# Performance work log

Hardware: AMD Instinct MI355X
Metric: run time of the kernel (lower is better)

Reference implementation:

```python
import jax, jax.numpy as jnp
import numpy as np

B, S_F, S_H, S_W = 1, 4, 32, 32
S = S_F * S_H * S_W            # 4096 video tokens
DIM, HEADS = 1536, 12
HD = DIM // HEADS              # 128
EPS = 1e-6


def _rope_angles(max_pos, dim_half):
    inv = 1.0 / (10000.0 ** (np.arange(dim_half, dtype=np.float32) / dim_half))
    return (np.arange(max_pos, dtype=np.float32)[:, None] * inv[None, :]).astype(np.float32)


def setup_inputs():
    key = jax.random.key(0)
    ks = jax.random.split(key, 6)
    w = lambda k: jax.random.normal(k, (DIM, DIM), jnp.float32) * (DIM ** -0.5)
    c = HD // 2
    f0, f1 = c - 2 * (c // 3), c // 3   # 22, 21 (Wan rope split for F/H/W)
    freqs = jnp.asarray(np.concatenate(
        [_rope_angles(1024, f0), _rope_angles(1024, f1), _rope_angles(1024, f1)], axis=1))
    return dict(
        x=jax.random.normal(ks[0], (B, S, DIM), jnp.float32),
        seq_lens=jnp.full((B,), S, jnp.int32),
        grid_sizes=jnp.array([[S_F, S_H, S_W]], jnp.int32),
        freqs=freqs,
        t=500,
        Wq=w(ks[1]), bq=jnp.zeros((DIM,), jnp.float32),
        Wk=w(ks[2]), bk=jnp.zeros((DIM,), jnp.float32),
        Wv=w(ks[3]), bv=jnp.zeros((DIM,), jnp.float32),
        Wo=w(ks[4]), bo=jnp.zeros((DIM,), jnp.float32),
        gq=jnp.ones((DIM,), jnp.float32),
        gk=jnp.ones((DIM,), jnp.float32),
    )


def _rmsnorm(x, g):
    return x * jax.lax.rsqrt(jnp.mean(x * x, axis=-1, keepdims=True) + EPS) * g


def _rope_apply(x, cos, sin):
    # x: [B,S,n,d]; cos/sin: [S, d//2]; rotate interleaved (even, odd) pairs
    b, s, n, d = x.shape
    xr = x.reshape(b, s, n, d // 2, 2)
    xe, xo = xr[..., 0], xr[..., 1]
    c = cos[None, :, None, :]
    sn = sin[None, :, None, :]
    return jnp.stack([xe * c - xo * sn, xe * sn + xo * c], axis=-1).reshape(b, s, n, d)


def _rope_tables(grid_sizes, freqs):
    F, H, W = [int(v) for v in np.asarray(grid_sizes)[0]]
    c = HD // 2
    f0, f1 = c - 2 * (c // 3), c // 3
    ang = jnp.concatenate([
        jnp.broadcast_to(freqs[:F, :f0][:, None, None, :], (F, H, W, f0)),
        jnp.broadcast_to(freqs[:H, f0:f0 + f1][None, :, None, :], (F, H, W, f1)),
        jnp.broadcast_to(freqs[:W, f0 + f1:][None, None, :, :], (F, H, W, f1)),
    ], axis=-1).reshape(F * H * W, c)  # [S, d//2]
    return jnp.cos(ang), jnp.sin(ang)


def reference(x, seq_lens, grid_sizes, freqs, t, Wq, bq, Wk, bk, Wv, bv, Wo, bo, gq, gk):
    b, s = x.shape[:2]
    cos, sin = _rope_tables(grid_sizes, freqs)

    q = _rmsnorm(x @ Wq.T + bq, gq).reshape(b, s, HEADS, HD)
    k = _rmsnorm(x @ Wk.T + bk, gk).reshape(b, s, HEADS, HD)
    v = (x @ Wv.T + bv).reshape(b, s, HEADS, HD)
    q = _rope_apply(q, cos, sin)
    k = _rope_apply(k, cos, sin)

    scores = jnp.einsum('bqhd,bkhd->bhqk', q, k) * (HD ** -0.5)  # [B,H,S,S]
    kmask = jnp.arange(s)[None, :] < seq_lens[:, None]           # varlen key mask
    scores = jnp.where(kmask[:, None, None, :], scores, -jnp.inf)
    attn = jax.nn.softmax(scores, axis=-1)
    out = jnp.einsum('bhqk,bkhd->bqhd', attn, v).reshape(b, s, DIM)
    return out @ Wo.T + bo
```

## Files before the change

kernel.cpp:

```cpp
#include <hip/hip_runtime.h>
#include <hip/hip_bf16.h>

#define S 4096
#define DIM 1536
#define HEADS 12
#define HD 128
#define CHALF 64
#define NQKV 4608

typedef unsigned short u16;
typedef unsigned int u32;
typedef __attribute__((ext_vector_type(8))) short bf16x8;
typedef __attribute__((ext_vector_type(4))) float f32x4;
typedef __attribute__((ext_vector_type(16))) float f32x16;

__device__ __forceinline__ u16 f2b(float f) {
    u32 u = __float_as_uint(f);
    u32 r = (u + 0x7fffu + ((u >> 16) & 1u)) >> 16;
    return (u16)r;
}
__device__ __forceinline__ float b2f(u16 b) {
    return __uint_as_float(((u32)b) << 16);
}
__device__ __forceinline__ u32 pack2(float a, float b) {
    u32 lo = (__float_as_uint(a) + 0x8000u) >> 16;
    u32 hi = (__float_as_uint(b) + 0x8000u) & 0xffff0000u;
    return lo | hi;
}
__device__ __forceinline__ void gld_lds16(const u16* g, u16* l) {
    __builtin_amdgcn_global_load_lds((const __attribute__((address_space(1))) void*)g,
                                     (__attribute__((address_space(3))) void*)l, 16, 0, 0);
}

__global__ void k_cvt_all(const float4* __restrict__ x, const float4* __restrict__ wq,
                          const float4* __restrict__ wk, const float4* __restrict__ wv,
                          const float4* __restrict__ wo,
                          ushort4* __restrict__ xb, ushort4* __restrict__ wqkv,
                          ushort4* __restrict__ wob,
                          const float* __restrict__ freqs, const int* __restrict__ grid_sizes,
                          float* __restrict__ cosT, float* __restrict__ sinT) {
    const int N4X = S * DIM / 4, N4W = DIM * DIM / 4;
    const int NCVT = N4X + 4 * N4W;
    int i = blockIdx.x * 256 + threadIdx.x;
    if (i < NCVT) {
        const float4* src; ushort4* dst; int off;
        if (i < N4X) { src = x; dst = xb; off = i; }
        else {
            int j = i - N4X;
            int w = j / N4W; off = j - w * N4W;
            if (w == 0)      { src = wq; dst = wqkv; }
            else if (w == 1) { src = wk; dst = wqkv + N4W; }
            else if (w == 2) { src = wv; dst = wqkv + 2 * N4W; }
            else             { src = wo; dst = wob; }
        }
        float4 v = src[off];
        ushort4 o;
        o.x = f2b(v.x); o.y = f2b(v.y); o.z = f2b(v.z); o.w = f2b(v.w);
        dst[off] = o;
    } else {
        int idx = i - NCVT;
        int s = idx >> 6;
        int ii = idx & 63;
        int H = grid_sizes[1], W = grid_sizes[2];
        int hw = H * W;
        int f = s / hw;
        int rem = s - f * hw;
        int h = rem / W;
        int w = rem - h * W;
        const int f0 = 22, f1 = 21;
        int pos = (ii < f0) ? f : ((ii < f0 + f1) ? h : w);
        float ang = freqs[pos * CHALF + ii];
        cosT[idx] = cosf(ang);
        sinT[idx] = sinf(ang);
    }
}

template<int TN, int OUT_BF16, int QKV>
__global__ __launch_bounds__(256, 2) void k_gemm(const u16* __restrict__ A, const u16* __restrict__ W,
                                                 const float* __restrict__ b0, const float* __restrict__ b1,
                                                 const float* __restrict__ b2,
                                                 void* __restrict__ Cout, int N, int K, int ldc) {
    __shared__ u16 As[128 * 32];
    __shared__ u16 Bs[TN * 32];
    int tid = threadIdx.x;
    int lane = tid & 63, wave = tid >> 6;
    int quad = lane >> 4, l16 = lane & 15;
    int rowBase = blockIdx.y * 128;
    int colBase = blockIdx.x * TN;
    int lr = lane >> 2, lc = (lane & 3) << 3;

    constexpr int MI = (TN == 128) ? 4 : 2;
    int wm = (TN == 128) ? (wave >> 1) : wave;
    int wn = (TN == 128) ? (wave & 1) : 0;

    f32x4 acc[MI][4] = {};

    for (int kb = 0; kb < K; kb += 32) {
        __syncthreads();
        if (TN == 128) {
#pragma unroll
            for (int c = 0; c < 2; c++) {
                int rrel = wave * 32 + c * 16;
                gld_lds16(A + (size_t)(rowBase + rrel + lr) * K + kb + lc, As + rrel * 32);
                gld_lds16(W + (size_t)(colBase + rrel + lr) * K + kb + lc, Bs + rrel * 32);
            }
        } else {
            gld_lds16(A + (size_t)(rowBase + wave * 32 + lr) * K + kb + lc, As + (wave * 32) * 32);
            gld_lds16(A + (size_t)(rowBase + wave * 32 + 16 + lr) * K + kb + lc, As + (wave * 32 + 16) * 32);
            gld_lds16(W + (size_t)(colBase + wave * 16 + lr) * K + kb + lc, Bs + (wave * 16) * 32);
        }
        __syncthreads();

        bf16x8 a[MI], b[4];
#pragma unroll
        for (int mi = 0; mi < MI; mi++) {
            int row = (TN == 128) ? (wm * 64 + mi * 16 + l16) : (wave * 32 + mi * 16 + l16);
            a[mi] = *(const bf16x8*)(As + row * 32 + quad * 8);
        }
#pragma unroll
        for (int ni = 0; ni < 4; ni++) {
            int row = (TN == 128) ? (wn * 64 + ni * 16 + l16) : (ni * 16 + l16);
            b[ni] = *(const bf16x8*)(Bs + row * 32 + quad * 8);
        }
#pragma unroll
        for (int mi = 0; mi < MI; mi++)
#pragma unroll
            for (int ni = 0; ni < 4; ni++)
                acc[mi][ni] = __builtin_amdgcn_mfma_f32_16x16x32_bf16(a[mi], b[ni], acc[mi][ni], 0, 0, 0);
    }

#pragma unroll
    for (int mi = 0; mi < MI; mi++) {
#pragma unroll
        for (int ni = 0; ni < 4; ni++) {
            int col = colBase + ((TN == 128) ? wn * 64 : 0) + ni * 16 + l16;
            float bv;
            if (QKV) {
                int third = colBase / DIM;
                const float* bp = (third == 0) ? b0 : ((third == 1) ? b1 : b2);
                bv = bp[col - third * DIM];
            } else {
                bv = b0[col];
            }
#pragma unroll
            for (int r = 0; r < 4; r++) {
                int row = rowBase + ((TN == 128) ? wm * 64 : wave * 32) + mi * 16 + quad * 4 + r;
                float v = acc[mi][ni][r] + bv;
                if (OUT_BF16)
                    ((u16*)Cout)[(size_t)row * ldc + col] = f2b(v);
                else
                    ((float*)Cout)[(size_t)row * ldc + col] = v;
            }
        }
    }
}

__global__ __launch_bounds__(256) void k_normrope(u16* __restrict__ qkvp, const float* __restrict__ gq,
                                                  const float* __restrict__ gk,
                                                  const float* __restrict__ cosT, const float* __restrict__ sinT,
                                                  float qscale) {
    int s = blockIdx.x;
    int which = blockIdx.y;
    const float* g = which ? gk : gq;
    float scale = which ? 1.0f : qscale;
    int tid = threadIdx.x;
    int lane = tid & 63, wave = tid >> 6;
    u32* row = (u32*)(qkvp + (size_t)s * NQKV + which * DIM);

    int w0 = tid, w1 = tid + 256, w2 = tid + 512;
    u32 p0 = row[w0], p1 = row[w1], p2 = row[w2];
    float e0 = b2f(p0 & 0xffff), o0 = b2f(p0 >> 16);
    float e1 = b2f(p1 & 0xffff), o1 = b2f(p1 >> 16);
    float e2 = b2f(p2 & 0xffff), o2 = b2f(p2 >> 16);
    float ss = e0 * e0 + o0 * o0 + e1 * e1 + o1 * o1 + e2 * e2 + o2 * o2;

    __shared__ float wsum[4];
    for (int off = 32; off; off >>= 1) ss += __shfl_down(ss, off);
    if (lane == 0) wsum[wave] = ss;
    __syncthreads();
    float tot = wsum[0] + wsum[1] + wsum[2] + wsum[3];
    float r = rsqrtf(tot * (1.0f / DIM) + 1e-6f) * scale;

    const float* cr = cosT + (size_t)s * CHALF;
    const float* sr = sinT + (size_t)s * CHALF;
#pragma unroll
    for (int j = 0; j < 3; j++) {
        int p = (j == 0) ? w0 : (j == 1) ? w1 : w2;
        float e = (j == 0) ? e0 : (j == 1) ? e1 : e2;
        float o = (j == 0) ? o0 : (j == 1) ? o1 : o2;
        int i = p & 63;
        float c = cr[i], sn = sr[i];
        e = e * r * g[2 * p];
        o = o * r * g[2 * p + 1];
        float ne = e * c - o * sn;
        float no = e * sn + o * c;
        row[p] = (u32)f2b(ne) | ((u32)f2b(no) << 16);
    }
}

__global__ void k_transpose(const u16* __restrict__ src, u16* __restrict__ dst) {
    __shared__ u16 t[32][33];
    int bx = blockIdx.x;
    int by = blockIdx.y;
    int tx = threadIdx.x, ty = threadIdx.y;
#pragma unroll
    for (int i = 0; i < 4; i++)
        t[ty + i * 8][tx] = src[(size_t)(by * 32 + ty + i * 8) * NQKV + bx * 32 + tx];
    __syncthreads();
    int txp = (tx & ~12) | ((tx & 4) << 1) | ((tx & 8) >> 1);
#pragma unroll
    for (int i = 0; i < 4; i++)
        dst[(size_t)(bx * 32 + ty + i * 8) * S + by * 32 + txp] = t[tx][ty + i * 8];
}

#define FM 16.5f
__global__ __launch_bounds__(256, 3) void k_attn(const u16* __restrict__ qkv, const u16* __restrict__ vt,
                                                 u16* __restrict__ O0, u16* __restrict__ O1,
                                                 float* __restrict__ lT,
                                                 const int* __restrict__ seq_lens) {
    int bx = blockIdx.x;
    int xcd = bx & 7, slot = bx >> 3;
    int hp = xcd * 3 + (slot >> 5);
    int h = (hp >= HEADS) ? hp - HEADS : hp;
    int p = (hp >= HEADS) ? 1 : 0;
    int q0 = (slot & 31) * 128;
    int kh0 = p * (S / 2);
    int tid = threadIdx.x;
    int lane = tid & 63, wave = tid >> 6;
    int l31 = lane & 31, hi = lane >> 5;
    int seqlen = seq_lens[0];
    u16* Op = p ? O1 : O0;

    __shared__ u16 Ks[64 * 136];
    __shared__ u16 Vs[128 * 88];

    int qrow = q0 + wave * 32 + l31;
    bf16x8 qf[8];
#pragma unroll
    for (int c = 0; c < 8; c++)
        qf[c] = *(const bf16x8*)(qkv + (size_t)qrow * NQKV + h * HD + c * 16 + hi * 8);

    f32x16 o_acc[4] = {};
    float lsum = 0.f;

    for (int kt = 0; kt < S / 2; kt += 64) {
        int kbase = kh0 + kt;
        __syncthreads();
        {
            int r = tid >> 2, cc = (tid & 3) * 32;
#pragma unroll
            for (int u = 0; u < 4; u++) {
                uint4 kv = *(const uint4*)(qkv + (size_t)(kbase + r) * NQKV + DIM + h * HD + cc + u * 8);
                *(uint4*)(Ks + r * 136 + cc + u * 8) = kv;
            }
            int dr = tid >> 3, dc = (tid & 7) * 8;
#pragma unroll
            for (int it = 0; it < 4; it++)
                *(uint4*)(Vs + (dr + it * 32) * 88 + dc) =
                    *(const uint4*)(vt + (size_t)(h * HD + dr + it * 32) * S + kbase + dc);
        }
        __syncthreads();

        f32x16 sc0 = {}, sc1 = {};
#pragma unroll
        for (int c = 0; c < 8; c++) {
            bf16x8 kf0 = *(const bf16x8*)(Ks + l31 * 136 + c * 16 + hi * 8);
            bf16x8 kf1 = *(const bf16x8*)(Ks + (32 + l31) * 136 + c * 16 + hi * 8);
            sc0 = __builtin_amdgcn_mfma_f32_32x32x16_bf16(kf0, qf[c], sc0, 0, 0, 0);
            sc1 = __builtin_amdgcn_mfma_f32_32x32x16_bf16(kf1, qf[c], sc1, 0, 0, 0);
        }

        bool tail = (kbase + 64 > seqlen);
        bf16x8 pfrag[4];
#pragma unroll
        for (int b = 0; b < 2; b++) {
            f32x16 s16 = b ? sc1 : sc0;
            u32 pk[4][2];
            if (!tail) {
#pragma unroll
                for (int g = 0; g < 4; g++) {
                    float e0 = __builtin_amdgcn_exp2f(s16[4 * g + 0]);
                    float e1 = __builtin_amdgcn_exp2f(s16[4 * g + 1]);
                    float e2 = __builtin_amdgcn_exp2f(s16[4 * g + 2]);
                    float e3 = __builtin_amdgcn_exp2f(s16[4 * g + 3]);
                    lsum += (e0 + e1) + (e2 + e3);
                    pk[g][0] = pack2(e0, e1);
                    pk[g][1] = pack2(e2, e3);
                }
            } else {
#pragma unroll
                for (int g = 0; g < 4; g++) {
                    float e[4];
#pragma unroll
                    for (int r = 0; r < 4; r++) {
                        int key = kbase + b * 32 + r + 8 * g + 4 * hi;
                        float v = __builtin_amdgcn_exp2f(s16[4 * g + r]);
                        e[r] = (key < seqlen) ? v : 0.f;
                        lsum += e[r];
                    }
                    pk[g][0] = pack2(e[0], e[1]);
                    pk[g][1] = pack2(e[2], e[3]);
                }
            }
            union { u32 u[4]; bf16x8 v; } c0v, c1v;
            c0v.u[0] = pk[0][0]; c0v.u[1] = pk[0][1]; c0v.u[2] = pk[1][0]; c0v.u[3] = pk[1][1];
            c1v.u[0] = pk[2][0]; c1v.u[1] = pk[2][1]; c1v.u[2] = pk[3][0]; c1v.u[3] = pk[3][1];
            pfrag[b * 2 + 0] = c0v.v;
            pfrag[b * 2 + 1] = c1v.v;
        }

#pragma unroll
        for (int db = 0; db < 4; db++) {
#pragma unroll
            for (int c4 = 0; c4 < 4; c4++) {
                bf16x8 vf = *(const bf16x8*)(Vs + (db * 32 + l31) * 88 + c4 * 16 + hi * 8);
                o_acc[db] = __builtin_amdgcn_mfma_f32_32x32x16_bf16(vf, pfrag[c4], o_acc[db], 0, 0, 0);
            }
        }
    }

    float l_all = lsum + __shfl_xor(lsum, 32);
    float linv = 1.0f / l_all;
#pragma unroll
    for (int db = 0; db < 4; db++) {
#pragma unroll
        for (int g = 0; g < 4; g++) {
            int d0 = db * 32 + 8 * g + 4 * hi;
            u16 o4[4];
#pragma unroll
            for (int r = 0; r < 4; r++)
                o4[r] = f2b(o_acc[db][4 * g + r] * linv);
            *(uint2*)(Op + (size_t)qrow * DIM + h * HD + d0) = *(const uint2*)o4;
        }
    }
    if (!hi) lT[((size_t)p * HEADS + h) * S + qrow] = l_all;
}

__global__ __launch_bounds__(384) void k_combine(u16* __restrict__ O0, const u16* __restrict__ O1,
                                                 const float* __restrict__ lT) {
    int q = blockIdx.x;
    int tid = threadIdx.x;
    int h = tid >> 5;
    size_t base = (size_t)q * DIM + tid * 4;
    float l0 = lT[(size_t)h * S + q];
    float l1 = lT[(size_t)(HEADS + h) * S + q];
    float inv = 1.0f / (l0 + l1);
    float c0 = l0 * inv, c1 = l1 * inv;
    uint2 u0 = *(const uint2*)(O0 + base);
    uint2 u1 = *(const uint2*)(O1 + base);
    const u16* a = (const u16*)&u0;
    const u16* b = (const u16*)&u1;
    u16 o[4];
#pragma unroll
    for (int i = 0; i < 4; i++)
        o[i] = f2b(c0 * b2f(a[i]) + c1 * b2f(b[i]));
    *(uint2*)(O0 + base) = *(uint2*)o;
}

extern "C" void kernel_launch(void* const* d_in, const int* in_sizes, int n_in,
                              void* d_out, int out_size, void* d_ws, size_t ws_size,
                              hipStream_t stream) {
    const float* x = (const float*)d_in[0];
    const int* seq_lens = (const int*)d_in[1];
    const int* grid_sizes = (const int*)d_in[2];
    const float* freqs = (const float*)d_in[3];
    const float* Wq = (const float*)d_in[5];
    const float* bq = (const float*)d_in[6];
    const float* Wk = (const float*)d_in[7];
    const float* bk = (const float*)d_in[8];
    const float* Wv = (const float*)d_in[9];
    const float* bv = (const float*)d_in[10];
    const float* Wo = (const float*)d_in[11];
    const float* bo = (const float*)d_in[12];
    const float* gq = (const float*)d_in[13];
    const float* gk = (const float*)d_in[14];
    float* out = (float*)d_out;

    char* w = (char*)d_ws;
    u16* xb    = (u16*)w; w += (size_t)S * DIM * 2;
    u16* qkv   = (u16*)w; w += (size_t)S * NQKV * 2;
    u16* Wqkvb = (u16*)w; w += (size_t)3 * DIM * DIM * 2;
    u16* Wob   = (u16*)w; w += (size_t)DIM * DIM * 2;
    u16* ab    = (u16*)w; w += (size_t)S * DIM * 2;
    u16* O1    = (u16*)w; w += (size_t)S * DIM * 2;
    float* cosT = (float*)w; w += (size_t)S * CHALF * 4;
    float* sinT = (float*)w; w += (size_t)S * CHALF * 4;
    float* lT  = (float*)w; w += (size_t)2 * HEADS * S * 4;
    u16* vt = Wqkvb;

    const float qscale = 0.08838834764831845f * 1.44269504088896341f;

    const int N4X = S * DIM / 4, N4W = DIM * DIM / 4;
    const int NCVT = N4X + 4 * N4W;
    const int NTAB = S * CHALF;
    k_cvt_all<<<(NCVT + NTAB) / 256, 256, 0, stream>>>(
        (const float4*)x, (const float4*)Wq, (const float4*)Wk, (const float4*)Wv, (const float4*)Wo,
        (ushort4*)xb, (ushort4*)Wqkvb, (ushort4*)Wob,
        freqs, grid_sizes, cosT, sinT);

    k_gemm<128, 1, 1><<<dim3(NQKV / 128, S / 128), 256, 0, stream>>>(
        xb, Wqkvb, bq, bk, bv, qkv, NQKV, DIM, NQKV);

    k_normrope<<<dim3(S, 2), 256, 0, stream>>>(qkv, gq, gk, cosT, sinT, qscale);

    k_transpose<<<dim3(DIM / 32, S / 32), dim3(32, 8), 0, stream>>>(qkv + 2 * DIM, vt);

    k_attn<<<dim3(768), 256, 0, stream>>>(qkv, vt, ab, O1, lT, seq_lens);

    k_combine<<<S, 384, 0, stream>>>(ab, O1, lT);

    k_gemm<64, 0, 0><<<dim3(DIM / 64, S / 128), 256, 0, stream>>>(
        ab, Wob, bo, bo, bo, out, DIM, DIM, DIM);
}
```

Before: 391.1 us.

## Use 32x32x16 MFMA with 64-wide K tiles and XOR-swizzled LDS in GEMM

Reworks the projection GEMM so each K step loads 64 elements instead of 32, halving the number of barrier pairs per tile. The inner product switches from 16x16x32 to 32x32x16 MFMA instructions, which cuts LDS fragment reads per FLOP. The LDS layout is XOR-swizzled by row to avoid bank conflicts on the wider rows. The cost is double the LDS footprint, which could reduce occupancy at the requested two blocks per CU, and a strided epilogue store pattern.

```diff
diff --git a/kernel.cpp b/kernel.cpp
--- a/kernel.cpp
+++ b/kernel.cpp
@@ -80,60 +80,63 @@
                                                  const float* __restrict__ b0, const float* __restrict__ b1,
                                                  const float* __restrict__ b2,
                                                  void* __restrict__ Cout, int N, int K, int ldc) {
-    __shared__ u16 As[128 * 32];
-    __shared__ u16 Bs[TN * 32];
+    __shared__ u16 As[128 * 64];
+    __shared__ u16 Bs[TN * 64];
     int tid = threadIdx.x;
     int lane = tid & 63, wave = tid >> 6;
-    int quad = lane >> 4, l16 = lane & 15;
+    int l31 = lane & 31, hi = lane >> 5;
     int rowBase = blockIdx.y * 128;
     int colBase = blockIdx.x * TN;
-    int lr = lane >> 2, lc = (lane & 3) << 3;
-
-    constexpr int MI = (TN == 128) ? 4 : 2;
-    int wm = (TN == 128) ? (wave >> 1) : wave;
-    int wn = (TN == 128) ? (wave & 1) : 0;
-
-    f32x4 acc[MI][4] = {};
-
-    for (int kb = 0; kb < K; kb += 32) {
+
+    int srow = lane >> 3;
+    int scol = (((lane & 7) ^ (srow & 7)) << 3);
+
+    constexpr int MI = (TN == 128) ? 2 : 1;
+    int rw = (TN == 128) ? ((wave >> 1) * 64) : (wave * 32);
+    int cw = (TN == 128) ? ((wave & 1) * 64) : 0;
+    int lx = l31 & 7;
+
+    f32x16 acc[MI][2] = {};
+
+    for (int kb = 0; kb < K; kb += 64) {
         __syncthreads();
-        if (TN == 128) {
-#pragma unroll
-            for (int c = 0; c < 2; c++) {
-                int rrel = wave * 32 + c * 16;
-                gld_lds16(A + (size_t)(rowBase + rrel + lr) * K + kb + lc, As + rrel * 32);
-                gld_lds16(W + (size_t)(colBase + rrel + lr) * K + kb + lc, Bs + rrel * 32);
-            }
-        } else {
-            gld_lds16(A + (size_t)(rowBase + wave * 32 + lr) * K + kb + lc, As + (wave * 32) * 32);
-            gld_lds16(A + (size_t)(rowBase + wave * 32 + 16 + lr) * K + kb + lc, As + (wave * 32 + 16) * 32);
-            gld_lds16(W + (size_t)(colBase + wave * 16 + lr) * K + kb + lc, Bs + (wave * 16) * 32);
+        {
+#pragma unroll
+            for (int it = 0; it < 4; it++) {
+                int rb = wave * 32 + it * 8;
+                gld_lds16(A + (size_t)(rowBase + rb + srow) * K + kb + scol, As + rb * 64);
+            }
+#pragma unroll
+            for (int it = 0; it < (TN == 128 ? 4 : 2); it++) {
+                int rb = wave * (TN == 128 ? 32 : 16) + it * 8;
+                gld_lds16(W + (size_t)(colBase + rb + srow) * K + kb + scol, Bs + rb * 64);
+            }
         }
         __syncthreads();
 
-        bf16x8 a[MI], b[4];
-#pragma unroll
-        for (int mi = 0; mi < MI; mi++) {
-            int row = (TN == 128) ? (wm * 64 + mi * 16 + l16) : (wave * 32 + mi * 16 + l16);
-            a[mi] = *(const bf16x8*)(As + row * 32 + quad * 8);
-        }
-#pragma unroll
-        for (int ni = 0; ni < 4; ni++) {
-            int row = (TN == 128) ? (wn * 64 + ni * 16 + l16) : (ni * 16 + l16);
-            b[ni] = *(const bf16x8*)(Bs + row * 32 + quad * 8);
-        }
-#pragma unroll
-        for (int mi = 0; mi < MI; mi++)
-#pragma unroll
-            for (int ni = 0; ni < 4; ni++)
-                acc[mi][ni] = __builtin_amdgcn_mfma_f32_16x16x32_bf16(a[mi], b[ni], acc[mi][ni], 0, 0, 0);
+#pragma unroll
+        for (int kk = 0; kk < 4; kk++) {
+            int chk = ((kk * 2 + hi) ^ lx) << 3;
+            bf16x8 af[MI], bf[2];
+#pragma unroll
+            for (int mi = 0; mi < MI; mi++)
+                af[mi] = *(const bf16x8*)(As + (rw + mi * 32 + l31) * 64 + chk);
+#pragma unroll
+            for (int ni = 0; ni < 2; ni++)
+                bf[ni] = *(const bf16x8*)(Bs + (cw + ni * 32 + l31) * 64 + chk);
+#pragma unroll
+            for (int mi = 0; mi < MI; mi++)
+#pragma unroll
+                for (int ni = 0; ni < 2; ni++)
+                    acc[mi][ni] = __builtin_amdgcn_mfma_f32_32x32x16_bf16(af[mi], bf[ni], acc[mi][ni], 0, 0, 0);
+        }
     }
 
 #pragma unroll
     for (int mi = 0; mi < MI; mi++) {
 #pragma unroll
-        for (int ni = 0; ni < 4; ni++) {
-            int col = colBase + ((TN == 128) ? wn * 64 : 0) + ni * 16 + l16;
+        for (int ni = 0; ni < 2; ni++) {
+            int col = colBase + cw + ni * 32 + l31;
             float bv;
             if (QKV) {
                 int third = colBase / DIM;
@@ -143,9 +146,9 @@
                 bv = b0[col];
             }
 #pragma unroll
-            for (int r = 0; r < 4; r++) {
-                int row = rowBase + ((TN == 128) ? wm * 64 : wave * 32) + mi * 16 + quad * 4 + r;
-                float v = acc[mi][ni][r] + bv;
+            for (int g = 0; g < 16; g++) {
+                int row = rowBase + rw + mi * 32 + (g & 3) + 8 * (g >> 2) + 4 * hi;
+                float v = acc[mi][ni][g] + bv;
                 if (OUT_BF16)
                     ((u16*)Cout)[(size_t)row * ldc + col] = f2b(v);
                 else
@@ -213,7 +216,6 @@
         dst[(size_t)(bx * 32 + ty + i * 8) * S + by * 32 + txp] = t[tx][ty + i * 8];
 }
 
-#define FM 16.5f
 __global__ __launch_bounds__(256, 3) void k_attn(const u16* __restrict__ qkv, const u16* __restrict__ vt,
                                                  u16* __restrict__ O0, u16* __restrict__ O1,
                                                  float* __restrict__ lT,
```

Result: faster. 372.8 us, median of 2 (-4.7%).
